# Performance work log

Measured on AMD Instinct MI355X. Metric: run time of the kernel, lower is better.

## Reference

```python
import jax, jax.numpy as jnp
import numpy as np

NX, NY, NZ = 64, 48, 32          # grid_resolution
N = NX * NY * NZ                 # 98304 grid cells
P = 10                           # neighbors_in_radius
D = 3                            # spatial dims
M = 5                            # num_modes (fourier)
BN = 64                          # base_neurons
BN_IN = 8                        # base_neurons_in (output channels)
IN_FEAT = D * (1 + 2 * M)        # 33


def _linear_init(k, fan_in, fan_out):
    s = 1.0 / np.sqrt(fan_in)
    kw, kb = jax.random.split(k)
    W = jax.random.uniform(kw, (fan_in, fan_out), jnp.float32, -s, s)
    b = jax.random.uniform(kb, (fan_out,), jnp.float32, -s, s)
    return W, b


def setup_inputs() -> dict:
    key = jax.random.key(0)
    ks = jax.random.split(key, 6)
    # neighbor point coordinates gathered by ball query: (b, N, P, 3)
    x = jax.random.normal(ks[0], (1, N, P, D), jnp.float32)
    # regular grid coordinates: (b, nx, ny, nz, 3)
    grid = jax.random.normal(ks[1], (1, NX, NY, NZ, D), jnp.float32)
    # fourier frequency buffer: exp(linspace(0, pi, num_modes))
    freqs = jnp.exp(jnp.linspace(0.0, float(np.pi), M)).astype(jnp.float32)
    W1, b1 = _linear_init(ks[2], IN_FEAT, BN)
    W2, b2 = _linear_init(ks[3], BN, BN // 2)
    W3, b3 = _linear_init(ks[4], BN // 2, BN_IN)
    return dict(x=x, grid=grid, freqs=freqs,
                W1=W1, b1=b1, W2=W2, b2=b2, W3=W3, b3=b3)


def _fourier_encode(coords, freqs):
    # coords: (b, N, P, D), freqs: (F,)
    scaled = coords[..., None, :] * freqs[:, None]          # (b, N, P, F, D)
    b, n, p = coords.shape[:3]
    scaled = scaled.reshape(b, n, p, -1)                    # (b, N, P, F*D)
    return jnp.concatenate([jnp.sin(scaled), jnp.cos(scaled)], axis=-1)


def reference(x, grid, freqs, W1, b1, W2, b2, W3, b3):
    gelu = lambda t: jax.nn.gelu(t, approximate=False)  # torch F.gelu default = exact erf
    # Fourier feature encode neighbor coords: (b, N, P, 33)
    facets = jnp.concatenate([x, _fourier_encode(x, freqs)], axis=-1)
    h = gelu(facets @ W1 + b1)                              # (b, N, P, 64)
    h = gelu(h @ W2 + b2)                                   # (b, N, P, 32)
    h = jnp.tanh(h @ W3 + b3)                               # (b, N, P, 8)
    # mask out padded neighbors (zero coords); original uses x-coordinate channel
    mask = (jnp.abs(x[..., 0:1]) > 1e-6).astype(h.dtype)    # (b, N, P, 1)
    out = jnp.sum(h * mask, axis=2)                         # scatter/aggregate -> (b, N, 8)
    out = out.reshape(out.shape[0], NX, NY, NZ, BN_IN)
    return jnp.transpose(out, (0, 4, 1, 2, 3))              # (b, 8, nx, ny, nz)
```

## Files before the change

kernel.cpp:

```cpp
#include <hip/hip_runtime.h>
#include <math.h>

#define NXD 64
#define NYD 48
#define NZD 32
#define NPT (NXD*NYD*NZD)
#define PN  10
#define MF  5
#define H1  64
#define H2  32
#define H3  8

#define PTS_PER_BLOCK 32
#define ROWS_PER_BLOCK (PTS_PER_BLOCK*PN)
#define TILES_PER_WAVE 5

#define A2S 72
#define A3S 40

typedef __attribute__((ext_vector_type(8))) short short8;
typedef __attribute__((ext_vector_type(4))) float f32x4;

__device__ __forceinline__ short f2bf(float f) {
    unsigned u = __float_as_uint(f);
    unsigned r = (u + 0x7fffu + ((u >> 16) & 1u)) >> 16;
    return (short)r;
}

__device__ __forceinline__ unsigned short f2bf_hu(float f) {
    return (unsigned short)((__float_as_uint(f) + 0x8000u) >> 16);
}

__device__ __forceinline__ unsigned pack2_bf16(float lo, float hi) {
    return __builtin_amdgcn_perm(__float_as_uint(hi) + 0x8000u,
                                 __float_as_uint(lo) + 0x8000u, 0x07060302u);
}

__device__ __forceinline__ float gelu_fast(float x) {
    float x2 = x * x;
    float t  = x * (1.59576912f + 0.07135482f * x2);
    float E  = __expf(t);
    return x - x * __builtin_amdgcn_rcpf(E + 1.0f);
}

__device__ __forceinline__ float tanh_fast(float v) {
    float E = __expf(2.0f * v);
    return 1.0f - 2.0f * __builtin_amdgcn_rcpf(E + 1.0f);
}

__global__ __launch_bounds__(256) void domino_mfma_kernel(
    const float* __restrict__ x,
    const float* __restrict__ freqs,
    const float* __restrict__ W1,
    const float* __restrict__ b1,
    const float* __restrict__ W2,
    const float* __restrict__ b2,
    const float* __restrict__ W3,
    const float* __restrict__ b3,
    float* __restrict__ out)
{
    __shared__ float obuf[ROWS_PER_BLOCK * 9];
    __shared__ __align__(16) unsigned short a2buf[4][16 * A2S];
    __shared__ __align__(16) unsigned short a3buf[4][16 * A3S];
    __shared__ __align__(16) float mcx[4][16];
    __shared__ __align__(16) float mv32[4][16];

    const int tid  = threadIdx.x;
    const int w    = tid >> 6;
    const int lane = tid & 63;
    const int lr   = lane & 15;
    const int lg   = lane >> 4;

    float fr[MF];
    #pragma unroll
    for (int m = 0; m < MF; ++m) fr[m] = freqs[m];

    short8 B1f[4];
    float  w32[4], bv1[4];
    #pragma unroll
    for (int t1 = 0; t1 < 4; ++t1) {
        #pragma unroll
        for (int j = 0; j < 8; ++j)
            B1f[t1][j] = f2bf(W1[(lg*8 + j)*H1 + t1*16 + lr]);
        w32[t1] = W1[32*H1 + t1*16 + lr];
        bv1[t1] = b1[t1*16 + lr];
    }
    short8 B2f[2][2];
    float  bv2[2];
    #pragma unroll
    for (int s = 0; s < 2; ++s)
        #pragma unroll
        for (int t2 = 0; t2 < 2; ++t2)
            #pragma unroll
            for (int j = 0; j < 8; ++j)
                B2f[s][t2][j] = f2bf(W2[(s*32 + lg*8 + j)*H2 + t2*16 + lr]);
    #pragma unroll
    for (int t2 = 0; t2 < 2; ++t2) bv2[t2] = b2[t2*16 + lr];

    short8 B3f;
    float  bv3 = (lr < H3) ? b3[lr] : 0.0f;
    #pragma unroll
    for (int j = 0; j < 8; ++j)
        B3f[j] = (lr < H3) ? f2bf(W3[(lg*8 + j)*H3 + lr]) : (short)0;

    const int wrow0 = blockIdx.x * ROWS_PER_BLOCK + w * (TILES_PER_WAVE*16);

    #pragma unroll 1
    for (int t = 0; t < TILES_PER_WAVE; ++t) {
        const int myrow = wrow0 + t*16 + lr;

        const float* xp = x + (size_t)myrow * 3;
        const float cx = xp[0], cy = xp[1], cz = xp[2];

        float sv[15], cv[15];
        #pragma unroll
        for (int m = 0; m < MF; ++m) {
            __sincosf(fr[m]*cx, &sv[m*3+0], &cv[m*3+0]);
            __sincosf(fr[m]*cy, &sv[m*3+1], &cv[m*3+1]);
            __sincosf(fr[m]*cz, &sv[m*3+2], &cv[m*3+2]);
        }

        if (lg == 0) { mcx[w][lr] = cx; mv32[w][lr] = cv[14]; }

        float fv[8];
        if (lg == 0) {
            fv[0]=cx; fv[1]=cy; fv[2]=cz;
            fv[3]=sv[0]; fv[4]=sv[1]; fv[5]=sv[2]; fv[6]=sv[3]; fv[7]=sv[4];
        } else if (lg == 1) {
            fv[0]=sv[5];  fv[1]=sv[6];  fv[2]=sv[7];  fv[3]=sv[8];
            fv[4]=sv[9];  fv[5]=sv[10]; fv[6]=sv[11]; fv[7]=sv[12];
        } else if (lg == 2) {
            fv[0]=sv[13]; fv[1]=sv[14]; fv[2]=cv[0];  fv[3]=cv[1];
            fv[4]=cv[2];  fv[5]=cv[3];  fv[6]=cv[4];  fv[7]=cv[5];
        } else {
            fv[0]=cv[6];  fv[1]=cv[7];  fv[2]=cv[8];  fv[3]=cv[9];
            fv[4]=cv[10]; fv[5]=cv[11]; fv[6]=cv[12]; fv[7]=cv[13];
        }
        union { unsigned u[4]; short8 s8; } a1u;
        #pragma unroll
        for (int j = 0; j < 4; ++j) a1u.u[j] = pack2_bf16(fv[2*j], fv[2*j+1]);
        const short8 a1 = a1u.s8;

        f32x4 c1[4];
        #pragma unroll
        for (int t1 = 0; t1 < 4; ++t1) {
            f32x4 ci = {bv1[t1], bv1[t1], bv1[t1], bv1[t1]};
            c1[t1] = __builtin_amdgcn_mfma_f32_16x16x32_bf16(a1, B1f[t1], ci, 0, 0, 0);
        }
        const f32x4 v32r = *(const f32x4*)&mv32[w][lg*4];
        const f32x4 mxr  = *(const f32x4*)&mcx[w][lg*4];
        #pragma unroll
        for (int t1 = 0; t1 < 4; ++t1)
            #pragma unroll
            for (int r = 0; r < 4; ++r)
                c1[t1][r] += v32r[r] * w32[t1];
        #pragma unroll
        for (int t1 = 0; t1 < 4; ++t1)
            #pragma unroll
            for (int r = 0; r < 4; ++r)
                c1[t1][r] = gelu_fast(c1[t1][r]);

        #pragma unroll
        for (int t1 = 0; t1 < 4; ++t1)
            #pragma unroll
            for (int r = 0; r < 4; ++r)
                a2buf[w][(lg*4 + r)*A2S + t1*16 + lr] = f2bf_hu(c1[t1][r]);
        short8 a2f[2];
        #pragma unroll
        for (int s = 0; s < 2; ++s)
            a2f[s] = *(const short8*)&a2buf[w][lr*A2S + s*32 + lg*8];

        f32x4 c2[2];
        #pragma unroll
        for (int t2 = 0; t2 < 2; ++t2) {
            f32x4 ci = {bv2[t2], bv2[t2], bv2[t2], bv2[t2]};
            ci = __builtin_amdgcn_mfma_f32_16x16x32_bf16(a2f[0], B2f[0][t2], ci, 0, 0, 0);
            c2[t2] = __builtin_amdgcn_mfma_f32_16x16x32_bf16(a2f[1], B2f[1][t2], ci, 0, 0, 0);
        }
        #pragma unroll
        for (int t2 = 0; t2 < 2; ++t2)
            #pragma unroll
            for (int r = 0; r < 4; ++r)
                c2[t2][r] = gelu_fast(c2[t2][r]);

        #pragma unroll
        for (int t2 = 0; t2 < 2; ++t2)
            #pragma unroll
            for (int r = 0; r < 4; ++r)
                a3buf[w][(lg*4 + r)*A3S + t2*16 + lr] = f2bf_hu(c2[t2][r]);
        short8 a3f = *(const short8*)&a3buf[w][lr*A3S + lg*8];

        f32x4 c3 = {bv3, bv3, bv3, bv3};
        c3 = __builtin_amdgcn_mfma_f32_16x16x32_bf16(a3f, B3f, c3, 0, 0, 0);

        #pragma unroll
        for (int r = 0; r < 4; ++r) {
            const int brow = w*(TILES_PER_WAVE*16) + t*16 + lg*4 + r;
            const float mk = (fabsf(mxr[r]) > 1e-6f) ? 1.0f : 0.0f;
            if (lr < H3) obuf[brow*9 + lr] = mk * tanh_fast(c3[r]);
        }
    }

    __syncthreads();

    {
        const int p  = tid >> 3;
        const int ch = tid & 7;
        float sum = 0.0f;
        #pragma unroll
        for (int i = 0; i < PN; ++i) sum += obuf[(p*PN + i)*9 + ch];
        const int gp = blockIdx.x * PTS_PER_BLOCK + p;
        out[(size_t)ch * NPT + gp] = sum;
    }
}

extern "C" void kernel_launch(void* const* d_in, const int* in_sizes, int n_in,
                              void* d_out, int out_size, void* d_ws, size_t ws_size,
                              hipStream_t stream) {
    const float* x     = (const float*)d_in[0];
    const float* freqs = (const float*)d_in[2];
    const float* W1    = (const float*)d_in[3];
    const float* b1    = (const float*)d_in[4];
    const float* W2    = (const float*)d_in[5];
    const float* b2    = (const float*)d_in[6];
    const float* W3    = (const float*)d_in[7];
    const float* b3    = (const float*)d_in[8];
    float* out = (float*)d_out;

    const int grid = NPT / PTS_PER_BLOCK;
    domino_mfma_kernel<<<grid, 256, 0, stream>>>(x, freqs, W1, b1, W2, b2, W3, b3, out);
}
```

Before: 127.2 us.

## Compute only needed Fourier features per lane via permuted W1 rows and hardware sin

Each 16-lane group now evaluates just the 8 sin/cos features it feeds into the MFMA A-fragment, using a slot table that remaps W1 rows so the features can be ordered arbitrarily. Cos is computed as sin with a quarter-turn offset via v_sin on fract(revolutions), replacing 30 sincos calls per lane with 8 hardware sines. GELU and tanh switch to exp2 with pre-scaled constants. This cuts redundant transcendental work; it relies on the low-precision hardware sin and on the table being correct.

```diff
diff --git a/kernel.cpp b/kernel.cpp
--- a/kernel.cpp
+++ b/kernel.cpp
@@ -18,8 +18,16 @@
 #define A2S 72
 #define A3S 40
 
+#define INV2PI 0.15915494309189535f
+
 typedef __attribute__((ext_vector_type(8))) short short8;
 typedef __attribute__((ext_vector_type(4))) float f32x4;
+
+static __device__ const unsigned short kSlotTab[32] = {
+  2048,    3,   70,  137,  204,  271, 1042, 1109,
+  2561, 1176, 1243, 1310,  516,  583,  650,  717,
+  2562,  272, 1043, 1110, 1177, 1244, 1311,  517,
+    72,  139,  206,  273, 1044, 1111, 1178, 1245 };
 
 __device__ __forceinline__ short f2bf(float f) {
     unsigned u = __float_as_uint(f);
@@ -38,13 +46,13 @@
 
 __device__ __forceinline__ float gelu_fast(float x) {
     float x2 = x * x;
-    float t  = x * (1.59576912f + 0.07135482f * x2);
-    float E  = __expf(t);
+    float t  = x * (2.3022082f + 0.10294324f * x2);
+    float E  = __builtin_amdgcn_exp2f(t);
     return x - x * __builtin_amdgcn_rcpf(E + 1.0f);
 }
 
 __device__ __forceinline__ float tanh_fast(float v) {
-    float E = __expf(2.0f * v);
+    float E = __builtin_amdgcn_exp2f(2.8853901f * v);
     return 1.0f - 2.0f * __builtin_amdgcn_rcpf(E + 1.0f);
 }
 
@@ -71,9 +79,26 @@
     const int lr   = lane & 15;
     const int lg   = lane >> 4;
 
-    float fr[MF];
-    #pragma unroll
-    for (int m = 0; m < MF; ++m) fr[m] = freqs[m];
+    float fA[8], fB[8], offs[8];
+    int   rowidx[8];
+    float f4rev;
+    {
+        float fr[MF];
+        #pragma unroll
+        for (int m = 0; m < MF; ++m) fr[m] = freqs[m];
+        f4rev = fr[4] * INV2PI;
+        #pragma unroll
+        for (int j = 0; j < 8; ++j) {
+            const unsigned e = kSlotTab[lg*8 + j];
+            const int row = e & 63, m = (e >> 6) & 7, path = (e >> 9) & 1, ty = (e >> 10) & 3;
+            rowidx[j] = row;
+            const float fm = fr[m] * INV2PI;
+            fA[j]   = (ty != 2 && path == 0) ? fm : 0.0f;
+            fB[j]   = (ty != 2 && path == 1) ? fm : 0.0f;
+            offs[j] = (ty == 1) ? 0.25f : 0.0f;
+        }
+    }
+    const float rawf = (lg < 3) ? 1.0f : 0.0f;
 
     short8 B1f[4];
     float  w32[4], bv1[4];
@@ -81,7 +106,7 @@
     for (int t1 = 0; t1 < 4; ++t1) {
         #pragma unroll
         for (int j = 0; j < 8; ++j)
-            B1f[t1][j] = f2bf(W1[(lg*8 + j)*H1 + t1*16 + lr]);
+            B1f[t1][j] = f2bf(W1[rowidx[j]*H1 + t1*16 + lr]);
         w32[t1] = W1[32*H1 + t1*16 + lr];
         bv1[t1] = b1[t1*16 + lr];
     }
@@ -112,30 +137,22 @@
         const float* xp = x + (size_t)myrow * 3;
         const float cx = xp[0], cy = xp[1], cz = xp[2];
 
-        float sv[15], cv[15];
-        #pragma unroll
-        for (int m = 0; m < MF; ++m) {
-            __sincosf(fr[m]*cx, &sv[m*3+0], &cv[m*3+0]);
-            __sincosf(fr[m]*cy, &sv[m*3+1], &cv[m*3+1]);
-            __sincosf(fr[m]*cz, &sv[m*3+2], &cv[m*3+2]);
-        }
-
-        if (lg == 0) { mcx[w][lr] = cx; mv32[w][lr] = cv[14]; }
+        const float cA = (lg <= 1) ? cx : ((lg == 2) ? cy : cz);
+        const float cB = (lg == 0) ? cx : ((lg == 1) ? cy : cz);
 
         float fv[8];
+        #pragma unroll
+        for (int j = 0; j < 8; ++j) {
+            float rev = cA * fA[j] + (cB * fB[j] + offs[j]);
+            fv[j] = __builtin_amdgcn_sinf(__builtin_amdgcn_fractf(rev));
+        }
+        fv[0] += rawf * (cB - fv[0]);
+
         if (lg == 0) {
-            fv[0]=cx; fv[1]=cy; fv[2]=cz;
-            fv[3]=sv[0]; fv[4]=sv[1]; fv[5]=sv[2]; fv[6]=sv[3]; fv[7]=sv[4];
-        } else if (lg == 1) {
-            fv[0]=sv[5];  fv[1]=sv[6];  fv[2]=sv[7];  fv[3]=sv[8];
-            fv[4]=sv[9];  fv[5]=sv[10]; fv[6]=sv[11]; fv[7]=sv[12];
-        } else if (lg == 2) {
-            fv[0]=sv[13]; fv[1]=sv[14]; fv[2]=cv[0];  fv[3]=cv[1];
-            fv[4]=cv[2];  fv[5]=cv[3];  fv[6]=cv[4];  fv[7]=cv[5];
-        } else {
-            fv[0]=cv[6];  fv[1]=cv[7];  fv[2]=cv[8];  fv[3]=cv[9];
-            fv[4]=cv[10]; fv[5]=cv[11]; fv[6]=cv[12]; fv[7]=cv[13];
-        }
+            mcx[w][lr]  = cx;
+            mv32[w][lr] = __builtin_amdgcn_sinf(__builtin_amdgcn_fractf(cz * f4rev + 0.25f));
+        }
+
         union { unsigned u[4]; short8 s8; } a1u;
         #pragma unroll
         for (int j = 0; j < 4; ++j) a1u.u[j] = pack2_bf16(fv[2*j], fv[2*j+1]);
```

Result: no change. 129.2 us (+1.6%).
